# Performance work log

Hardware: AMD Instinct MI355X
Metric: run time of the kernel (lower is better)

Reference implementation:

```python
import jax, jax.numpy as jnp
import numpy as np

B, D = 16384, 512          # batch, outer_dim
S = R = O = X = Y = Z = 64  # inner tensor-network ranks


def _xavier(key, shape):
    fan_in, fan_out = shape[-2], shape[-1]
    if len(shape) == 3:
        fan_in = shape[0] * shape[1]
        fan_out = shape[2]
    limit = float(np.sqrt(6.0 / (fan_in + fan_out)))
    return jax.random.uniform(key, shape, jnp.float32, -limit, limit)


def setup_inputs() -> dict:
    key = jax.random.key(0)
    ks = jax.random.split(key, 12)
    return {
        "input1": jax.random.normal(ks[0], (B, D), jnp.float32),
        "input2": jax.random.normal(ks[1], (B, D), jnp.float32),
        "input3": jax.random.normal(ks[2], (B, D), jnp.float32),
        "proj_s": _xavier(ks[3], (D, S)),
        "proj_r": _xavier(ks[4], (R, R)),   # first_param = inn_r since with_nn
        "proj_o": _xavier(ks[5], (D, O)),
        "cube_s": _xavier(ks[6], (S, Y, Z)),
        "cube_r": _xavier(ks[7], (X, R, Z)),
        "cube_o": _xavier(ks[8], (X, Y, O)),
        "W21": _xavier(ks[9], (R, D)),
        "b21": jnp.zeros((R,), jnp.float32),
        "W22": _xavier(ks[10], (R, R)),
        "b22": jnp.zeros((R,), jnp.float32),
        "W23": _xavier(ks[11], (R, R)),
        "b23": jnp.zeros((R,), jnp.float32),
    }


def reference(input1, input2, input3, proj_s, proj_r, proj_o,
              cube_s, cube_r, cube_o, W21, b21, W22, b22, W23, b23):
    # relation MLP (with_nn=True branch)
    h = jax.nn.relu(input2 @ W21.T + b21)
    h = jax.nn.relu(h @ W22.T + b22)
    h = h @ W23.T + b23
    # projections: einsum('Ss,bS->bs', proj, x) == x @ proj
    p1 = input1 @ proj_s   # [B, S]
    p2 = h @ proj_r        # [B, R]
    p3 = input3 @ proj_o   # [B, O]
    # triangle contraction 'bs,br,bo,syz,xrz,xyo->b', contracted efficiently
    a = jnp.einsum('bs,syz->byz', p1, cube_s)
    b = jnp.einsum('br,xrz->bxz', p2, cube_r)
    c = jnp.einsum('bo,xyo->bxy', p3, cube_o)
    return jnp.einsum('byz,bxz,bxy->b', a, b, c)
```

## Files before the change

kernel.cpp:

```cpp
#include <hip/hip_runtime.h>
#include <hip/hip_bf16.h>
#include <cstdint>
#include <cstddef>


typedef __attribute__((ext_vector_type(8))) short short8;
typedef __attribute__((ext_vector_type(4))) float f32x4;

#define DEV static __device__ __forceinline__

constexpr int NB = 16384;
constexpr int ND = 512;

DEV unsigned short f2bf(float f) {
    union { float f; unsigned u; } v; v.f = f;
    unsigned r = v.u + 0x7FFFu + ((v.u >> 16) & 1u);
    return (unsigned short)(r >> 16);
}
DEV float bf2f(unsigned short h) {
    union { unsigned u; float f; } v; v.u = ((unsigned)h) << 16;
    return v.f;
}
DEV unsigned swz(unsigned byte_addr, int row) {
    return byte_addr ^ ((unsigned)(row & 7) << 4);
}

__global__ void k_prep(const float* __restrict__ proj_s, const float* __restrict__ proj_r,
                       const float* __restrict__ proj_o, const float* __restrict__ cube_s,
                       const float* __restrict__ cube_r, const float* __restrict__ cube_o,
                       const float* __restrict__ W21, const float* __restrict__ W22,
                       const float* __restrict__ W23,
                       unsigned short* __restrict__ Wp1t, unsigned short* __restrict__ Wh1,
                       unsigned short* __restrict__ Wp3t, unsigned short* __restrict__ W22b,
                       unsigned short* __restrict__ W23b, unsigned short* __restrict__ Prt,
                       unsigned short* __restrict__ csb, unsigned short* __restrict__ crb,
                       unsigned short* __restrict__ cot)
{
    int i = blockIdx.x * 256 + threadIdx.x;
    if (i < 32768) { int d = i >> 6, s = i & 63; Wp1t[s * 512 + d] = f2bf(proj_s[i]); return; }
    i -= 32768;
    if (i < 32768) { Wh1[i] = f2bf(W21[i]); return; }
    i -= 32768;
    if (i < 32768) { int d = i >> 6, o = i & 63; Wp3t[o * 512 + d] = f2bf(proj_o[i]); return; }
    i -= 32768;
    if (i < 4096) { W22b[i] = f2bf(W22[i]); return; }
    i -= 4096;
    if (i < 4096) { W23b[i] = f2bf(W23[i]); return; }
    i -= 4096;
    if (i < 4096) { int k = i >> 6, n = i & 63; Prt[n * 64 + k] = f2bf(proj_r[i]); return; }
    i -= 4096;
    if (i < 262144) { csb[i] = f2bf(cube_s[i]); return; }
    i -= 262144;
    if (i < 262144) { crb[i] = f2bf(cube_r[i]); return; }
    i -= 262144;
    if (i < 262144) { int x = i >> 12, y = (i >> 6) & 63, o = i & 63;
                      cot[o * 4096 + x * 64 + y] = f2bf(cube_o[i]); return; }
}

__global__ __launch_bounds__(256, 2) void k_proj(
    const float* __restrict__ in1, const float* __restrict__ in2, const float* __restrict__ in3,
    const unsigned short* __restrict__ Wp1t, const unsigned short* __restrict__ Wh1,
    const unsigned short* __restrict__ Wp3t, const float* __restrict__ b21,
    unsigned short* __restrict__ p1bf, unsigned short* __restrict__ hbf,
    unsigned short* __restrict__ p3bf)
{
    __shared__ __align__(16) unsigned short lds_w[64 * 512];
    __shared__ __align__(16) unsigned short lds_a[128 * 64];
    const int z = blockIdx.y;
    const float* in = (z == 0) ? in1 : (z == 1) ? in2 : in3;
    const unsigned short* Wt = (z == 0) ? Wp1t : (z == 1) ? Wh1 : Wp3t;
    unsigned short* outp = (z == 0) ? p1bf : (z == 1) ? hbf : p3bf;

    const int t = threadIdx.x;
    const int b0 = blockIdx.x * 128;

#pragma unroll
    for (int i = 0; i < 16; ++i) {
        int c = t + i * 256;
        int n = c >> 6, c16 = c & 63;
        uint4 v = *(const uint4*)(Wt + n * 512 + c16 * 8);
        *(uint4*)((char*)lds_w + swz(n * 1024 + c16 * 16, n)) = v;
    }
    const int wid = t >> 6, l = t & 63, lr = l & 15, lk = l >> 4;
    f32x4 acc[2][4] = {};
    for (int kc = 0; kc < 8; ++kc) {
#pragma unroll
        for (int i = 0; i < 4; ++i) {
            int u = t + i * 256;
            int row = u >> 3, e8 = u & 7;
            const float* src = in + (size_t)(b0 + row) * ND + kc * 64 + e8 * 8;
            float4 fa = *(const float4*)src;
            float4 fb = *(const float4*)(src + 4);
            uint4 pk;
            pk.x = (unsigned)f2bf(fa.x) | ((unsigned)f2bf(fa.y) << 16);
            pk.y = (unsigned)f2bf(fa.z) | ((unsigned)f2bf(fa.w) << 16);
            pk.z = (unsigned)f2bf(fb.x) | ((unsigned)f2bf(fb.y) << 16);
            pk.w = (unsigned)f2bf(fb.z) | ((unsigned)f2bf(fb.w) << 16);
            *(uint4*)((char*)lds_a + swz(row * 128 + e8 * 16, row)) = pk;
        }
        __syncthreads();
#pragma unroll
        for (int ks = 0; ks < 2; ++ks) {
            short8 av[2], bv[4];
#pragma unroll
            for (int f = 0; f < 2; ++f) {
                int row = wid * 32 + f * 16 + lr;
                av[f] = *(const short8*)((const char*)lds_a + swz(row * 128 + (ks * 32 + lk * 8) * 2, row));
            }
#pragma unroll
            for (int g = 0; g < 4; ++g) {
                int n = g * 16 + lr;
                bv[g] = *(const short8*)((const char*)lds_w + swz(n * 1024 + (kc * 64 + ks * 32 + lk * 8) * 2, n));
            }
#pragma unroll
            for (int f = 0; f < 2; ++f)
#pragma unroll
                for (int g = 0; g < 4; ++g)
                    acc[f][g] = __builtin_amdgcn_mfma_f32_16x16x32_bf16(av[f], bv[g], acc[f][g], 0, 0, 0);
        }
        __syncthreads();
    }
#pragma unroll
    for (int f = 0; f < 2; ++f)
#pragma unroll
        for (int g = 0; g < 4; ++g)
#pragma unroll
            for (int q = 0; q < 4; ++q) {
                int row = wid * 32 + f * 16 + lk * 4 + q;
                int col = g * 16 + lr;
                float v = acc[f][g][q];
                if (z == 1) v = fmaxf(v + b21[col], 0.0f);
                outp[(size_t)(b0 + row) * 64 + col] = f2bf(v);
            }
}

DEV void mlp_stage(const unsigned short* src_lds, const unsigned short* w_lds,
                   const float* __restrict__ bias, bool do_relu,
                   unsigned short* dst_lds, unsigned short* __restrict__ dst_g,
                   int b0, int wid, int lr, int lk)
{
    f32x4 acc[2][4] = {};
#pragma unroll
    for (int ks = 0; ks < 2; ++ks) {
        short8 av[2], bv[4];
#pragma unroll
        for (int f = 0; f < 2; ++f) {
            int row = wid * 32 + f * 16 + lr;
            av[f] = *(const short8*)((const char*)src_lds + swz(row * 128 + (ks * 32 + lk * 8) * 2, row));
        }
#pragma unroll
        for (int g = 0; g < 4; ++g) {
            int n = g * 16 + lr;
            bv[g] = *(const short8*)((const char*)w_lds + swz(n * 128 + (ks * 32 + lk * 8) * 2, n));
        }
#pragma unroll
        for (int f = 0; f < 2; ++f)
#pragma unroll
            for (int g = 0; g < 4; ++g)
                acc[f][g] = __builtin_amdgcn_mfma_f32_16x16x32_bf16(av[f], bv[g], acc[f][g], 0, 0, 0);
    }
#pragma unroll
    for (int f = 0; f < 2; ++f)
#pragma unroll
        for (int g = 0; g < 4; ++g)
#pragma unroll
            for (int q = 0; q < 4; ++q) {
                int row = wid * 32 + f * 16 + lk * 4 + q;
                int col = g * 16 + lr;
                float v = acc[f][g][q];
                if (bias) v += bias[col];
                if (do_relu) v = fmaxf(v, 0.0f);
                unsigned short hv = f2bf(v);
                if (dst_lds) *(unsigned short*)((char*)dst_lds + swz(row * 128 + col * 2, row)) = hv;
                else dst_g[(size_t)(b0 + row) * 64 + col] = hv;
            }
}

__global__ __launch_bounds__(256, 2) void k_mlp(
    const unsigned short* __restrict__ hbf,
    const unsigned short* __restrict__ W22b, const unsigned short* __restrict__ W23b,
    const unsigned short* __restrict__ Prt,
    const float* __restrict__ b22, const float* __restrict__ b23,
    unsigned short* __restrict__ p2bf)
{
    __shared__ __align__(16) unsigned short lds_w[3][64 * 64];
    __shared__ __align__(16) unsigned short lds_x[128 * 64];
    __shared__ __align__(16) unsigned short lds_y[128 * 64];
    const int t = threadIdx.x;
    const int b0 = blockIdx.x * 128;
#pragma unroll
    for (int i = 0; i < 6; ++i) {
        int c = t + i * 256;
        int w = c >> 9, cc = c & 511;
        int n = cc >> 3, c16 = cc & 7;
        const unsigned short* W = (w == 0) ? W22b : (w == 1) ? W23b : Prt;
        uint4 v = *(const uint4*)(W + n * 64 + c16 * 8);
        *(uint4*)((char*)lds_w[w] + swz(n * 128 + c16 * 16, n)) = v;
    }
#pragma unroll
    for (int i = 0; i < 4; ++i) {
        int u = t + i * 256;
        int row = u >> 3, c16 = u & 7;
        uint4 v = *(const uint4*)(hbf + (size_t)(b0 + row) * 64 + c16 * 8);
        *(uint4*)((char*)lds_x + swz(row * 128 + c16 * 16, row)) = v;
    }
    __syncthreads();
    const int wid = t >> 6, l = t & 63, lr = l & 15, lk = l >> 4;
    mlp_stage(lds_x, lds_w[0], b22, true,  lds_y, nullptr, b0, wid, lr, lk);
    __syncthreads();
    mlp_stage(lds_y, lds_w[1], b23, false, lds_x, nullptr, b0, wid, lr, lk);
    __syncthreads();
    mlp_stage(lds_x, lds_w[2], nullptr, false, nullptr, p2bf, b0, wid, lr, lk);
}

__global__ __launch_bounds__(256, 2) void k_F(
    const unsigned short* __restrict__ crb, const unsigned short* __restrict__ csb,
    unsigned short* __restrict__ F2)
{
    __shared__ __align__(16) unsigned short lds_a[128 * 64];
    __shared__ __align__(16) unsigned short lds_b[128 * 64];
    const int t = threadIdx.x;
    const int m0 = blockIdx.x * 128, n0 = blockIdx.y * 128;
#pragma unroll
    for (int i = 0; i < 4; ++i) {
        int u = t + i * 256;
        int row = u >> 3, c16 = u & 7;
        uint4 va = *(const uint4*)(crb + (size_t)(m0 + row) * 64 + c16 * 8);
        *(uint4*)((char*)lds_a + swz(row * 128 + c16 * 16, row)) = va;
        uint4 vb = *(const uint4*)(csb + (size_t)(n0 + row) * 64 + c16 * 8);
        *(uint4*)((char*)lds_b + swz(row * 128 + c16 * 16, row)) = vb;
    }
    __syncthreads();
    const int wid = t >> 6, l = t & 63, lr = l & 15, lk = l >> 4;
    const int wm = wid & 1, wn = wid >> 1;
    f32x4 acc[4][4] = {};
#pragma unroll
    for (int ks = 0; ks < 2; ++ks) {
        short8 av[4], bv[4];
#pragma unroll
        for (int f = 0; f < 4; ++f) {
            int row = wm * 64 + f * 16 + lr;
            av[f] = *(const short8*)((const char*)lds_a + swz(row * 128 + (ks * 32 + lk * 8) * 2, row));
            int col = wn * 64 + f * 16 + lr;
            bv[f] = *(const short8*)((const char*)lds_b + swz(col * 128 + (ks * 32 + lk * 8) * 2, col));
        }
#pragma unroll
        for (int f = 0; f < 4; ++f)
#pragma unroll
            for (int g = 0; g < 4; ++g)
                acc[f][g] = __builtin_amdgcn_mfma_f32_16x16x32_bf16(av[f], bv[g], acc[f][g], 0, 0, 0);
    }
#pragma unroll
    for (int f = 0; f < 4; ++f)
#pragma unroll
        for (int g = 0; g < 4; ++g)
#pragma unroll
            for (int q = 0; q < 4; ++q) {
                int row = m0 + wm * 64 + f * 16 + lk * 4 + q;
                int col = n0 + wn * 64 + g * 16 + lr;
                F2[(size_t)row * 4096 + col] = f2bf(acc[f][g][q]);
            }
}

__global__ __launch_bounds__(256, 1) void k_T(
    const unsigned short* __restrict__ F2, const unsigned short* __restrict__ cot,
    unsigned short* __restrict__ Tts)
{
    __shared__ __align__(16) unsigned short lds[4][2][64 * 64];
    const int s = blockIdx.x;
    const int t = threadIdx.x;
    const int wid = t >> 6, l = t & 63, lr = l & 15, lk = l >> 4;
    f32x4 acc[4][4] = {};
    for (int xi = 0; xi < 16; ++xi) {
        int x = wid * 16 + xi;
#pragma unroll
        for (int i = 0; i < 8; ++i) {
            int u = l + i * 64;
            int rr = u >> 3, c16 = u & 7;
            uint4 va = *(const uint4*)(F2 + (size_t)(x * 64 + rr) * 4096 + s * 64 + c16 * 8);
            *(uint4*)((char*)lds[wid][0] + swz(rr * 128 + c16 * 16, rr)) = va;
            uint4 vb = *(const uint4*)(cot + (size_t)rr * 4096 + x * 64 + c16 * 8);
            *(uint4*)((char*)lds[wid][1] + swz(rr * 128 + c16 * 16, rr)) = vb;
        }
        asm volatile("s_waitcnt lgkmcnt(0)" ::: "memory");
        __builtin_amdgcn_sched_barrier(0);
#pragma unroll
        for (int ks = 0; ks < 2; ++ks) {
            short8 av[4], bv[4];
#pragma unroll
            for (int f = 0; f < 4; ++f) {
                int rr = f * 16 + lr;
                av[f] = *(const short8*)((const char*)lds[wid][0] + swz(rr * 128 + (ks * 32 + lk * 8) * 2, rr));
                bv[f] = *(const short8*)((const char*)lds[wid][1] + swz(rr * 128 + (ks * 32 + lk * 8) * 2, rr));
            }
#pragma unroll
            for (int f = 0; f < 4; ++f)
#pragma unroll
                for (int g = 0; g < 4; ++g)
                    acc[f][g] = __builtin_amdgcn_mfma_f32_16x16x32_bf16(av[f], bv[g], acc[f][g], 0, 0, 0);
        }
    }
    __syncthreads();
    float* red = (float*)&lds[0][0][0];
#pragma unroll
    for (int f = 0; f < 4; ++f)
#pragma unroll
        for (int g = 0; g < 4; ++g)
#pragma unroll
            for (int q = 0; q < 4; ++q) {
                int r = f * 16 + lk * 4 + q;
                int o = g * 16 + lr;
                red[wid * 4096 + r * 64 + o] = acc[f][g][q];
            }
    __syncthreads();
#pragma unroll
    for (int i = 0; i < 16; ++i) {
        int idx = t + i * 256;
        float v = red[idx] + red[4096 + idx] + red[8192 + idx] + red[12288 + idx];
        Tts[(size_t)s * 4096 + idx] = f2bf(v);
    }
}

__global__ __launch_bounds__(256, 2) void k_main(
    const unsigned short* __restrict__ p1bf, const unsigned short* __restrict__ p2bf,
    const unsigned short* __restrict__ p3bf, const unsigned short* __restrict__ Tts,
    float* __restrict__ out)
{
    __shared__ __align__(16) unsigned short lds_t[64 * 64];
    __shared__ __align__(16) unsigned short lds_p2[128 * 64];
    __shared__ __align__(16) unsigned short lds_p3[128 * 64];
    const int t = threadIdx.x;
    const int b0 = blockIdx.x * 128;
    const int kh = blockIdx.y;
#pragma unroll
    for (int i = 0; i < 4; ++i) {
        int u = t + i * 256;
        int row = u >> 3, c16 = u & 7;
        uint4 v2 = *(const uint4*)(p2bf + (size_t)(b0 + row) * 64 + c16 * 8);
        *(uint4*)((char*)lds_p2 + swz(row * 128 + c16 * 16, row)) = v2;
        uint4 v3 = *(const uint4*)(p3bf + (size_t)(b0 + row) * 64 + c16 * 8);
        *(uint4*)((char*)lds_p3 + swz(row * 128 + c16 * 16, row)) = v3;
    }
    __syncthreads();
    const int wid = t >> 6, l = t & 63, lr = l & 15, lk = l >> 4;
    float p3v[2][2][8];
#pragma unroll
    for (int f = 0; f < 2; ++f)
#pragma unroll
        for (int ks = 0; ks < 2; ++ks) {
            int row = wid * 32 + f * 16 + lr;
            short8 v = *(const short8*)((const char*)lds_p3 + swz(row * 128 + (ks * 32 + lk * 8) * 2, row));
#pragma unroll
            for (int j = 0; j < 8; ++j) p3v[f][ks][j] = bf2f((unsigned short)v[j]);
        }
    f32x4 acc[2][4] = {};
    for (int kc = kh * 32; kc < kh * 32 + 32; ++kc) {
#pragma unroll
        for (int i = 0; i < 2; ++i) {
            int u = t + i * 256;
            int srow = u >> 3, c16 = u & 7;
            uint4 v = *(const uint4*)(Tts + (size_t)srow * 4096 + kc * 64 + c16 * 8);
            *(uint4*)((char*)lds_t + swz(srow * 128 + c16 * 16, srow)) = v;
        }
        __syncthreads();
        float p2v[2];
#pragma unroll
        for (int f = 0; f < 2; ++f) {
            int row = wid * 32 + f * 16 + lr;
            p2v[f] = bf2f(*(const unsigned short*)((const char*)lds_p2 + swz(row * 128 + kc * 2, row)));
        }
#pragma unroll
        for (int ks = 0; ks < 2; ++ks) {
            short8 av[2], bv[4];
#pragma unroll
            for (int f = 0; f < 2; ++f) {
                short8 a;
#pragma unroll
                for (int j = 0; j < 8; ++j) a[j] = (short)f2bf(p2v[f] * p3v[f][ks][j]);
                av[f] = a;
            }
#pragma unroll
            for (int g = 0; g < 4; ++g) {
                int n = g * 16 + lr;
                bv[g] = *(const short8*)((const char*)lds_t + swz(n * 128 + (ks * 32 + lk * 8) * 2, n));
            }
#pragma unroll
            for (int f = 0; f < 2; ++f)
#pragma unroll
                for (int g = 0; g < 4; ++g)
                    acc[f][g] = __builtin_amdgcn_mfma_f32_16x16x32_bf16(av[f], bv[g], acc[f][g], 0, 0, 0);
        }
        __syncthreads();
    }
    float rsum[2][4] = {};
#pragma unroll
    for (int f = 0; f < 2; ++f)
#pragma unroll
        for (int g = 0; g < 4; ++g)
#pragma unroll
            for (int q = 0; q < 4; ++q) {
                int row = wid * 32 + f * 16 + lk * 4 + q;
                int col = g * 16 + lr;
                float p1v = bf2f(p1bf[(size_t)(b0 + row) * 64 + col]);
                rsum[f][q] += acc[f][g][q] * p1v;
            }
#pragma unroll
    for (int f = 0; f < 2; ++f)
#pragma unroll
        for (int q = 0; q < 4; ++q) {
            float v = rsum[f][q];
            v += __shfl_xor(v, 1);
            v += __shfl_xor(v, 2);
            v += __shfl_xor(v, 4);
            v += __shfl_xor(v, 8);
            if (lr == 0) {
                int row = wid * 32 + f * 16 + lk * 4 + q;
                atomicAdd(&out[b0 + row], v);
            }
        }
}

extern "C" void kernel_launch(void* const* d_in, const int* in_sizes, int n_in,
                              void* d_out, int out_size, void* d_ws, size_t ws_size,
                              hipStream_t stream)
{
    const float* in1    = (const float*)d_in[0];
    const float* in2    = (const float*)d_in[1];
    const float* in3    = (const float*)d_in[2];
    const float* proj_s = (const float*)d_in[3];
    const float* proj_r = (const float*)d_in[4];
    const float* proj_o = (const float*)d_in[5];
    const float* cube_s = (const float*)d_in[6];
    const float* cube_r = (const float*)d_in[7];
    const float* cube_o = (const float*)d_in[8];
    const float* W21    = (const float*)d_in[9];
    const float* b21    = (const float*)d_in[10];
    const float* W22    = (const float*)d_in[11];
    const float* b22    = (const float*)d_in[12];
    const float* W23    = (const float*)d_in[13];
    const float* b23    = (const float*)d_in[14];
    float* out = (float*)d_out;

    char* ws = (char*)d_ws;
    size_t off = 0;
    auto alloc = [&](size_t bytes) -> char* {
        char* p = ws + off;
        off += (bytes + 255) & ~(size_t)255;
        return p;
    };
    unsigned short* p1bf = (unsigned short*)alloc((size_t)NB * 64 * 2);
    unsigned short* hbf  = (unsigned short*)alloc((size_t)NB * 64 * 2);
    unsigned short* p2bf = (unsigned short*)alloc((size_t)NB * 64 * 2);
    unsigned short* p3bf = (unsigned short*)alloc((size_t)NB * 64 * 2);
    unsigned short* Wp1t = (unsigned short*)alloc(64 * 512 * 2);
    unsigned short* Wh1  = (unsigned short*)alloc(64 * 512 * 2);
    unsigned short* Wp3t = (unsigned short*)alloc(64 * 512 * 2);
    unsigned short* W22b = (unsigned short*)alloc(64 * 64 * 2);
    unsigned short* W23b = (unsigned short*)alloc(64 * 64 * 2);
    unsigned short* Prt  = (unsigned short*)alloc(64 * 64 * 2);
    unsigned short* csb  = (unsigned short*)alloc(262144 * 2);
    unsigned short* crb  = (unsigned short*)alloc(262144 * 2);
    unsigned short* cot  = (unsigned short*)alloc(262144 * 2);
    unsigned short* Tts  = (unsigned short*)alloc(64 * 4096 * 2);
    unsigned short* F2   = (unsigned short*)alloc((size_t)4096 * 4096 * 2);

    hipMemsetAsync(d_out, 0, (size_t)out_size * sizeof(float), stream);

    k_prep<<<3504, 256, 0, stream>>>(proj_s, proj_r, proj_o, cube_s, cube_r, cube_o,
                                     W21, W22, W23,
                                     Wp1t, Wh1, Wp3t, W22b, W23b, Prt, csb, crb, cot);
    k_proj<<<dim3(NB / 128, 3), 256, 0, stream>>>(in1, in2, in3, Wp1t, Wh1, Wp3t, b21,
                                                  p1bf, hbf, p3bf);
    k_mlp<<<NB / 128, 256, 0, stream>>>(hbf, W22b, W23b, Prt, b22, b23, p2bf);
    k_F<<<dim3(32, 32), 256, 0, stream>>>(crb, csb, F2);
    k_T<<<64, 256, 0, stream>>>(F2, cot, Tts);
    k_main<<<dim3(NB / 128, 2), 256, 0, stream>>>(p1bf, p2bf, p3bf, Tts, out);
}
```

Measured before the change: 236.0 us.

## Fuse MLP into projection kernel, split T across x-chunks, double-buffer main kernel

```diff
diff --git a/kernel.cpp b/kernel.cpp
--- a/kernel.cpp
+++ b/kernel.cpp
@@ -21,19 +21,24 @@
     union { unsigned u; float f; } v; v.u = ((unsigned)h) << 16;
     return v.f;
 }
-DEV unsigned swz(unsigned byte_addr, int row) {
-    return byte_addr ^ ((unsigned)(row & 7) << 4);
+DEV unsigned pack2(float lo, float hi) {
+    return (unsigned)f2bf(lo) | ((unsigned)f2bf(hi) << 16);
+}
+DEV short8 ldA_f32(const float* p) {
+    float4 a = *(const float4*)p, b = *(const float4*)(p + 4);
+    union { unsigned u[4]; short8 s; } v;
+    v.u[0] = pack2(a.x, a.y); v.u[1] = pack2(a.z, a.w);
+    v.u[2] = pack2(b.x, b.y); v.u[3] = pack2(b.z, b.w);
+    return v.s;
 }
 
 __global__ void k_prep(const float* __restrict__ proj_s, const float* __restrict__ proj_r,
-                       const float* __restrict__ proj_o, const float* __restrict__ cube_s,
-                       const float* __restrict__ cube_r, const float* __restrict__ cube_o,
+                       const float* __restrict__ proj_o, const float* __restrict__ cube_o,
                        const float* __restrict__ W21, const float* __restrict__ W22,
                        const float* __restrict__ W23,
                        unsigned short* __restrict__ Wp1t, unsigned short* __restrict__ Wh1,
                        unsigned short* __restrict__ Wp3t, unsigned short* __restrict__ W22b,
                        unsigned short* __restrict__ W23b, unsigned short* __restrict__ Prt,
-                       unsigned short* __restrict__ csb, unsigned short* __restrict__ crb,
                        unsigned short* __restrict__ cot)
 {
     int i = blockIdx.x * 256 + threadIdx.x;
@@ -49,375 +54,267 @@
     i -= 4096;
     if (i < 4096) { int k = i >> 6, n = i & 63; Prt[n * 64 + k] = f2bf(proj_r[i]); return; }
     i -= 4096;
-    if (i < 262144) { csb[i] = f2bf(cube_s[i]); return; }
-    i -= 262144;
-    if (i < 262144) { crb[i] = f2bf(cube_r[i]); return; }
-    i -= 262144;
     if (i < 262144) { int x = i >> 12, y = (i >> 6) & 63, o = i & 63;
                       cot[o * 4096 + x * 64 + y] = f2bf(cube_o[i]); return; }
+}
+
+__global__ __launch_bounds__(256, 2) void k_F(
+    const float* __restrict__ cr, const float* __restrict__ cs,
+    unsigned short* __restrict__ F2)
+{
+    const int t = threadIdx.x, wid = t >> 6, l = t & 63, lr = l & 15, lk = l >> 4;
+    const int wm = wid & 1, wn = wid >> 1;
+    const int m0 = blockIdx.x * 128 + wm * 64, n0 = blockIdx.y * 128 + wn * 64;
+    f32x4 acc[4][4] = {};
+#pragma unroll
+    for (int ks = 0; ks < 2; ++ks) {
+        short8 av[4], bv[4];
+#pragma unroll
+        for (int f = 0; f < 4; ++f) {
+            av[f] = ldA_f32(cr + (size_t)(m0 + f * 16 + lr) * 64 + ks * 32 + lk * 8);
+            bv[f] = ldA_f32(cs + (size_t)(n0 + f * 16 + lr) * 64 + ks * 32 + lk * 8);
+        }
+#pragma unroll
+        for (int f = 0; f < 4; ++f)
+#pragma unroll
+            for (int g = 0; g < 4; ++g)
+                acc[f][g] = __builtin_amdgcn_mfma_f32_16x16x32_bf16(av[f], bv[g], acc[f][g], 0, 0, 0);
+    }
+#pragma unroll
+    for (int f = 0; f < 4; ++f)
+#pragma unroll
+        for (int g = 0; g < 4; ++g)
+#pragma unroll
+            for (int q = 0; q < 4; ++q)
+                F2[(size_t)(m0 + f * 16 + lk * 4 + q) * 4096 + n0 + g * 16 + lr] = f2bf(acc[f][g][q]);
+}
+
+DEV void mlp_mm(const unsigned short* slab_w, const unsigned short* __restrict__ W,
+                int lr, int lk, f32x4 acc[4])
+{
+#pragma unroll
+    for (int ks = 0; ks < 2; ++ks) {
+        short8 av = *(const short8*)((const char*)slab_w +
+                      (lr * 128 + ((ks * 64 + lk * 16) ^ ((lr & 7) << 4))));
+#pragma unroll
+        for (int g = 0; g < 4; ++g) {
+            short8 bv = *(const short8*)(W + (g * 16 + lr) * 64 + ks * 32 + lk * 8);
+            acc[g] = __builtin_amdgcn_mfma_f32_16x16x32_bf16(av, bv, acc[g], 0, 0, 0);
+        }
+    }
+}
+DEV void store_slab(unsigned short* slab_w, int lr, int lk, const f32x4 acc[4],
+                    const float* __restrict__ bias, bool relu_)
+{
+#pragma unroll
+    for (int g = 0; g < 4; ++g) {
+        float bcol = bias ? bias[g * 16 + lr] : 0.0f;
+#pragma unroll
+        for (int q = 0; q < 4; ++q) {
+            int r = lk * 4 + q, c = g * 16 + lr;
+            float v = acc[g][q] + bcol;
+            if (relu_) v = fmaxf(v, 0.0f);
+            *(unsigned short*)((char*)slab_w + (r * 128 + ((c * 2) ^ ((r & 7) << 4)))) = f2bf(v);
+        }
+    }
 }
 
 __global__ __launch_bounds__(256, 2) void k_proj(
     const float* __restrict__ in1, const float* __restrict__ in2, const float* __restrict__ in3,
     const unsigned short* __restrict__ Wp1t, const unsigned short* __restrict__ Wh1,
-    const unsigned short* __restrict__ Wp3t, const float* __restrict__ b21,
-    unsigned short* __restrict__ p1bf, unsigned short* __restrict__ hbf,
+    const unsigned short* __restrict__ Wp3t,
+    const unsigned short* __restrict__ W22b, const unsigned short* __restrict__ W23b,
+    const unsigned short* __restrict__ Prt,
+    const float* __restrict__ b21, const float* __restrict__ b22, const float* __restrict__ b23,
+    unsigned short* __restrict__ p1bf, unsigned short* __restrict__ p2bf,
     unsigned short* __restrict__ p3bf)
 {
-    __shared__ __align__(16) unsigned short lds_w[64 * 512];
-    __shared__ __align__(16) unsigned short lds_a[128 * 64];
+    __shared__ __align__(16) unsigned short slab[4][1024];
     const int z = blockIdx.y;
     const float* in = (z == 0) ? in1 : (z == 1) ? in2 : in3;
     const unsigned short* Wt = (z == 0) ? Wp1t : (z == 1) ? Wh1 : Wp3t;
-    unsigned short* outp = (z == 0) ? p1bf : (z == 1) ? hbf : p3bf;
-
-    const int t = threadIdx.x;
-    const int b0 = blockIdx.x * 128;
-
-#pragma unroll
-    for (int i = 0; i < 16; ++i) {
-        int c = t + i * 256;
-        int n = c >> 6, c16 = c & 63;
-        uint4 v = *(const uint4*)(Wt + n * 512 + c16 * 8);
-        *(uint4*)((char*)lds_w + swz(n * 1024 + c16 * 16, n)) = v;
-    }
-    const int wid = t >> 6, l = t & 63, lr = l & 15, lk = l >> 4;
-    f32x4 acc[2][4] = {};
+    const int t = threadIdx.x, wid = t >> 6, l = t & 63, lr = l & 15, lk = l >> 4;
+    const int rbase = blockIdx.x * 64 + wid * 16;
+    const float* arow = in + (size_t)(rbase + lr) * ND;
+
+    f32x4 acc[4] = {};
+#pragma unroll
     for (int kc = 0; kc < 8; ++kc) {
 #pragma unroll
-        for (int i = 0; i < 4; ++i) {
-            int u = t + i * 256;
-            int row = u >> 3, e8 = u & 7;
-            const float* src = in + (size_t)(b0 + row) * ND + kc * 64 + e8 * 8;
-            float4 fa = *(const float4*)src;
-            float4 fb = *(const float4*)(src + 4);
-            uint4 pk;
-            pk.x = (unsigned)f2bf(fa.x) | ((unsigned)f2bf(fa.y) << 16);
-            pk.y = (unsigned)f2bf(fa.z) | ((unsigned)f2bf(fa.w) << 16);
-            pk.z = (unsigned)f2bf(fb.x) | ((unsigned)f2bf(fb.y) << 16);
-            pk.w = (unsigned)f2bf(fb.z) | ((unsigned)f2bf(fb.w) << 16);
-            *(uint4*)((char*)lds_a + swz(row * 128 + e8 * 16, row)) = pk;
-        }
+        for (int ks = 0; ks < 2; ++ks) {
+            short8 av = ldA_f32(arow + kc * 64 + ks * 32 + lk * 8);
+#pragma unroll
+            for (int g = 0; g < 4; ++g) {
+                short8 bv = *(const short8*)(Wt + (size_t)(g * 16 + lr) * 512 + kc * 64 + ks * 32 + lk * 8);
+                acc[g] = __builtin_amdgcn_mfma_f32_16x16x32_bf16(av, bv, acc[g], 0, 0, 0);
+            }
+        }
+    }
+    if (z != 1) {
+        unsigned short* outp = (z == 0) ? p1bf : p3bf;
+#pragma unroll
+        for (int g = 0; g < 4; ++g)
+#pragma unroll
+            for (int q = 0; q < 4; ++q)
+                outp[(size_t)(rbase + lk * 4 + q) * 64 + g * 16 + lr] = f2bf(acc[g][q]);
+    } else {
+        unsigned short* slw = slab[wid];
+        store_slab(slw, lr, lk, acc, b21, true);
         __syncthreads();
+        f32x4 a2[4] = {}; mlp_mm(slw, W22b, lr, lk, a2);
+        store_slab(slw, lr, lk, a2, b22, true);
+        __syncthreads();
+        f32x4 a3[4] = {}; mlp_mm(slw, W23b, lr, lk, a3);
+        store_slab(slw, lr, lk, a3, b23, false);
+        __syncthreads();
+        f32x4 a4[4] = {}; mlp_mm(slw, Prt, lr, lk, a4);
+#pragma unroll
+        for (int g = 0; g < 4; ++g)
+#pragma unroll
+            for (int q = 0; q < 4; ++q)
+                p2bf[(size_t)(rbase + lk * 4 + q) * 64 + g * 16 + lr] = f2bf(a4[g][q]);
+    }
+}
+
+__global__ __launch_bounds__(256, 2) void k_T(
+    const unsigned short* __restrict__ F2, const unsigned short* __restrict__ cot,
+    float* __restrict__ Tf)
+{
+    __shared__ float red[4][4096];
+    const int s = blockIdx.x, xh = blockIdx.y;
+    const int t = threadIdx.x, wid = t >> 6, l = t & 63, lr = l & 15, lk = l >> 4;
+    f32x4 acc[4][4] = {};
+#pragma unroll
+    for (int xi = 0; xi < 4; ++xi) {
+        int x = xh * 16 + wid * 4 + xi;
 #pragma unroll
         for (int ks = 0; ks < 2; ++ks) {
-            short8 av[2], bv[4];
-#pragma unroll
-            for (int f = 0; f < 2; ++f) {
-                int row = wid * 32 + f * 16 + lr;
-                av[f] = *(const short8*)((const char*)lds_a + swz(row * 128 + (ks * 32 + lk * 8) * 2, row));
+            short8 av[4], bv[4];
+#pragma unroll
+            for (int f = 0; f < 4; ++f) {
+                av[f] = *(const short8*)(F2 + (size_t)(x * 64 + f * 16 + lr) * 4096 + s * 64 + ks * 32 + lk * 8);
+                bv[f] = *(const short8*)(cot + (size_t)(f * 16 + lr) * 4096 + x * 64 + ks * 32 + lk * 8);
             }
 #pragma unroll
-            for (int g = 0; g < 4; ++g) {
-                int n = g * 16 + lr;
-                bv[g] = *(const short8*)((const char*)lds_w + swz(n * 1024 + (kc * 64 + ks * 32 + lk * 8) * 2, n));
-            }
-#pragma unroll
-            for (int f = 0; f < 2; ++f)
+            for (int f = 0; f < 4; ++f)
 #pragma unroll
                 for (int g = 0; g < 4; ++g)
                     acc[f][g] = __builtin_amdgcn_mfma_f32_16x16x32_bf16(av[f], bv[g], acc[f][g], 0, 0, 0);
         }
-        __syncthreads();
-    }
-#pragma unroll
-    for (int f = 0; f < 2; ++f)
+    }
+#pragma unroll
+    for (int f = 0; f < 4; ++f)
 #pragma unroll
         for (int g = 0; g < 4; ++g)
 #pragma unroll
-            for (int q = 0; q < 4; ++q) {
-                int row = wid * 32 + f * 16 + lk * 4 + q;
-                int col = g * 16 + lr;
-                float v = acc[f][g][q];
-                if (z == 1) v = fmaxf(v + b21[col], 0.0f);
-                outp[(size_t)(b0 + row) * 64 + col] = f2bf(v);
-            }
-}
-
-DEV void mlp_stage(const unsigned short* src_lds, const unsigned short* w_lds,
-                   const float* __restrict__ bias, bool do_relu,
-                   unsigned short* dst_lds, unsigned short* __restrict__ dst_g,
-                   int b0, int wid, int lr, int lk)
-{
-    f32x4 acc[2][4] = {};
-#pragma unroll
-    for (int ks = 0; ks < 2; ++ks) {
-        short8 av[2], bv[4];
-#pragma unroll
-        for (int f = 0; f < 2; ++f) {
-            int row = wid * 32 + f * 16 + lr;
-            av[f] = *(const short8*)((const char*)src_lds + swz(row * 128 + (ks * 32 + lk * 8) * 2, row));
-        }
-#pragma unroll
-        for (int g = 0; g < 4; ++g) {
-            int n = g * 16 + lr;
-            bv[g] = *(const short8*)((const char*)w_lds + swz(n * 128 + (ks * 32 + lk * 8) * 2, n));
-        }
-#pragma unroll
-        for (int f = 0; f < 2; ++f)
-#pragma unroll
-            for (int g = 0; g < 4; ++g)
-                acc[f][g] = __builtin_amdgcn_mfma_f32_16x16x32_bf16(av[f], bv[g], acc[f][g], 0, 0, 0);
-    }
-#pragma unroll
-    for (int f = 0; f < 2; ++f)
-#pragma unroll
-        for (int g = 0; g < 4; ++g)
-#pragma unroll
-            for (int q = 0; q < 4; ++q) {
-                int row = wid * 32 + f * 16 + lk * 4 + q;
-                int col = g * 16 + lr;
-                float v = acc[f][g][q];
-                if (bias) v += bias[col];
-                if (do_relu) v = fmaxf(v, 0.0f);
-                unsigned short hv = f2bf(v);
-                if (dst_lds) *(unsigned short*)((char*)dst_lds + swz(row * 128 + col * 2, row)) = hv;
-                else dst_g[(size_t)(b0 + row) * 64 + col] = hv;
-            }
-}
-
-__global__ __launch_bounds__(256, 2) void k_mlp(
-    const unsigned short* __restrict__ hbf,
-    const unsigned short* __restrict__ W22b, const unsigned short* __restrict__ W23b,
-    const unsigned short* __restrict__ Prt,
-    const float* __restrict__ b22, const float* __restrict__ b23,
-    unsigned short* __restrict__ p2bf)
-{
-    __shared__ __align__(16) unsigned short lds_w[3][64 * 64];
-    __shared__ __align__(16) unsigned short lds_x[128 * 64];
-    __shared__ __align__(16) unsigned short lds_y[128 * 64];
-    const int t = threadIdx.x;
-    const int b0 = blockIdx.x * 128;
-#pragma unroll
-    for (int i = 0; i < 6; ++i) {
-        int c = t + i * 256;
-        int w = c >> 9, cc = c & 511;
-        int n = cc >> 3, c16 = cc & 7;
-        const unsigned short* W = (w == 0) ? W22b : (w == 1) ? W23b : Prt;
-        uint4 v = *(const uint4*)(W + n * 64 + c16 * 8);
-        *(uint4*)((char*)lds_w[w] + swz(n * 128 + c16 * 16, n)) = v;
-    }
-#pragma unroll
-    for (int i = 0; i < 4; ++i) {
-        int u = t + i * 256;
-        int row = u >> 3, c16 = u & 7;
-        uint4 v = *(const uint4*)(hbf + (size_t)(b0 + row) * 64 + c16 * 8);
-        *(uint4*)((char*)lds_x + swz(row * 128 + c16 * 16, row)) = v;
-    }
-    __syncthreads();
-    const int wid = t >> 6, l = t & 63, lr = l & 15, lk = l >> 4;
-    mlp_stage(lds_x, lds_w[0], b22, true,  lds_y, nullptr, b0, wid, lr, lk);
-    __syncthreads();
-    mlp_stage(lds_y, lds_w[1], b23, false, lds_x, nullptr, b0, wid, lr, lk);
-    __syncthreads();
-    mlp_stage(lds_x, lds_w[2], nullptr, false, nullptr, p2bf, b0, wid, lr, lk);
-}
-
-__global__ __launch_bounds__(256, 2) void k_F(
-    const unsigned short* __restrict__ crb, const unsigned short* __restrict__ csb,
-    unsigned short* __restrict__ F2)
-{
-    __shared__ __align__(16) unsigned short lds_a[128 * 64];
-    __shared__ __align__(16) unsigned short lds_b[128 * 64];
-    const int t = threadIdx.x;
-    const int m0 = blockIdx.x * 128, n0 = blockIdx.y * 128;
-#pragma unroll
-    for (int i = 0; i < 4; ++i) {
-        int u = t + i * 256;
-        int row = u >> 3, c16 = u & 7;
-        uint4 va = *(const uint4*)(crb + (size_t)(m0 + row) * 64 + c16 * 8);
-        *(uint4*)((char*)lds_a + swz(row * 128 + c16 * 16, row)) = va;
-        uint4 vb = *(const uint4*)(csb + (size_t)(n0 + row) * 64 + c16 * 8);
-        *(uint4*)((char*)lds_b + swz(row * 128 + c16 * 16, row)) = vb;
-    }
-    __syncthreads();
-    const int wid = t >> 6, l = t & 63, lr = l & 15, lk = l >> 4;
-    const int wm = wid & 1, wn = wid >> 1;
-    f32x4 acc[4][4] = {};
-#pragma unroll
-    for (int ks = 0; ks < 2; ++ks) {
-        short8 av[4], bv[4];
-#pragma unroll
-        for (int f = 0; f < 4; ++f) {
-            int row = wm * 64 + f * 16 + lr;
-            av[f] = *(const short8*)((const char*)lds_a + swz(row * 128 + (ks * 32 + lk * 8) * 2, row));
-            int col = wn * 64 + f * 16 + lr;
-            bv[f] = *(const short8*)((const char*)lds_b + swz(col * 128 + (ks * 32 + lk * 8) * 2, col));
-        }
-#pragma unroll
-        for (int f = 0; f < 4; ++f)
-#pragma unroll
-            for (int g = 0; g < 4; ++g)
-                acc[f][g] = __builtin_amdgcn_mfma_f32_16x16x32_bf16(av[f], bv[g], acc[f][g], 0, 0, 0);
-    }
-#pragma unroll
-    for (int f = 0; f < 4; ++f)
-#pragma unroll
-        for (int g = 0; g < 4; ++g)
-#pragma unroll
-            for (int q = 0; q < 4; ++q) {
-                int row = m0 + wm * 64 + f * 16 + lk * 4 + q;
-                int col = n0 + wn * 64 + g * 16 + lr;
-                F2[(size_t)row * 4096 + col] = f2bf(acc[f][g][q]);
-            }
-}
-
-__global__ __launch_bounds__(256, 1) void k_T(
-    const unsigned short* __restrict__ F2, const unsigned short* __restrict__ cot,
-    unsigned short* __restrict__ Tts)
-{
-    __shared__ __align__(16) unsigned short lds[4][2][64 * 64];
-    const int s = blockIdx.x;
-    const int t = threadIdx.x;
-    const int wid = t >> 6, l = t & 63, lr = l & 15, lk = l >> 4;
-    f32x4 acc[4][4] = {};
-    for (int xi = 0; xi < 16; ++xi) {
-        int x = wid * 16 + xi;
-#pragma unroll
-        for (int i = 0; i < 8; ++i) {
-            int u = l + i * 64;
-            int rr = u >> 3, c16 = u & 7;
-            uint4 va = *(const uint4*)(F2 + (size_t)(x * 64 + rr) * 4096 + s * 64 + c16 * 8);
-            *(uint4*)((char*)lds[wid][0] + swz(rr * 128 + c16 * 16, rr)) = va;
-            uint4 vb = *(const uint4*)(cot + (size_t)rr * 4096 + x * 64 + c16 * 8);
-            *(uint4*)((char*)lds[wid][1] + swz(rr * 128 + c16 * 16, rr)) = vb;
-        }
-        asm volatile("s_waitcnt lgkmcnt(0)" ::: "memory");
-        __builtin_amdgcn_sched_barrier(0);
-#pragma unroll
-        for (int ks = 0; ks < 2; ++ks) {
-            short8 av[4], bv[4];
-#pragma unroll
-            for (int f = 0; f < 4; ++f) {
-                int rr = f * 16 + lr;
-                av[f] = *(const short8*)((const char*)lds[wid][0] + swz(rr * 128 + (ks * 32 + lk * 8) * 2, rr));
-                bv[f] = *(const short8*)((const char*)lds[wid][1] + swz(rr * 128 + (ks * 32 + lk * 8) * 2, rr));
-            }
-#pragma unroll
-            for (int f = 0; f < 4; ++f)
-#pragma unroll
-                for (int g = 0; g < 4; ++g)
-                    acc[f][g] = __builtin_amdgcn_mfma_f32_16x16x32_bf16(av[f], bv[g], acc[f][g], 0, 0, 0);
-        }
-    }
-    __syncthreads();
-    float* red = (float*)&lds[0][0][0];
-#pragma unroll
-    for (int f = 0; f < 4; ++f)
-#pragma unroll
-        for (int g = 0; g < 4; ++g)
-#pragma unroll
-            for (int q = 0; q < 4; ++q) {
-                int r = f * 16 + lk * 4 + q;
-                int o = g * 16 + lr;
-                red[wid * 4096 + r * 64 + o] = acc[f][g][q];
-            }
+            for (int q = 0; q < 4; ++q)
+                red[wid][(f * 16 + lk * 4 + q) * 64 + g * 16 + lr] = acc[f][g][q];
     __syncthreads();
 #pragma unroll
     for (int i = 0; i < 16; ++i) {
         int idx = t + i * 256;
-        float v = red[idx] + red[4096 + idx] + red[8192 + idx] + red[12288 + idx];
-        Tts[(size_t)s * 4096 + idx] = f2bf(v);
-    }
-}
-
-__global__ __launch_bounds__(256, 2) void k_main(
+        atomicAdd(&Tf[(size_t)s * 4096 + idx],
+                  red[0][idx] + red[1][idx] + red[2][idx] + red[3][idx]);
+    }
+}
+
+__global__ void k_cast(const float* __restrict__ Tf, unsigned short* __restrict__ Tts)
+{
+    int i = blockIdx.x * 256 + threadIdx.x;
+#pragma unroll
+    for (int j = 0; j < 4; ++j) {
+        int e = i * 4 + j;
+        int s = e >> 12, k = e & 4095;
+        int kc = k >> 6, kloc = k & 63;
+        Tts[kc * 4096 + s * 64 + kloc] = f2bf(Tf[e]);
+    }
+}
+
+__global__ __launch_bounds__(256, 4) void k_main(
     const unsigned short* __restrict__ p1bf, const unsigned short* __restrict__ p2bf,
     const unsigned short* __restrict__ p3bf, const unsigned short* __restrict__ Tts,
     float* __restrict__ out)
 {
-    __shared__ __align__(16) unsigned short lds_t[64 * 64];
-    __shared__ __align__(16) unsigned short lds_p2[128 * 64];
-    __shared__ __align__(16) unsigned short lds_p3[128 * 64];
-    const int t = threadIdx.x;
-    const int b0 = blockIdx.x * 128;
-    const int kh = blockIdx.y;
-#pragma unroll
-    for (int i = 0; i < 4; ++i) {
-        int u = t + i * 256;
-        int row = u >> 3, c16 = u & 7;
-        uint4 v2 = *(const uint4*)(p2bf + (size_t)(b0 + row) * 64 + c16 * 8);
-        *(uint4*)((char*)lds_p2 + swz(row * 128 + c16 * 16, row)) = v2;
-        uint4 v3 = *(const uint4*)(p3bf + (size_t)(b0 + row) * 64 + c16 * 8);
-        *(uint4*)((char*)lds_p3 + swz(row * 128 + c16 * 16, row)) = v3;
-    }
-    __syncthreads();
-    const int wid = t >> 6, l = t & 63, lr = l & 15, lk = l >> 4;
-    float p3v[2][2][8];
-#pragma unroll
-    for (int f = 0; f < 2; ++f)
+    __shared__ __align__(16) unsigned short tb[2][4096];
+    const int t = threadIdx.x, wid = t >> 6, l = t & 63, lr = l & 15, lk = l >> 4;
+    const int b0 = blockIdx.x * 64, kh = blockIdx.y;
+    const int row = b0 + wid * 16 + lr;
+
+    float p3v[2][8];
+#pragma unroll
+    for (int ks = 0; ks < 2; ++ks) {
+        short8 v = *(const short8*)(p3bf + (size_t)row * 64 + ks * 32 + lk * 8);
+#pragma unroll
+        for (int j = 0; j < 8; ++j) p3v[ks][j] = bf2f((unsigned short)v[j]);
+    }
+    short8 p2r[2];
+#pragma unroll
+    for (int i = 0; i < 2; ++i)
+        p2r[i] = *(const short8*)(p2bf + (size_t)row * 64 + kh * 16 + i * 8);
+
+    const int srow_st = t >> 2, kb_st = (t & 3) * 32;
+    const unsigned swz0 = (unsigned)(kb_st ^ ((srow_st & 7) << 4));
+    const unsigned swz1 = (unsigned)((kb_st + 16) ^ ((srow_st & 7) << 4));
+
+    {
+        const uint4* src = (const uint4*)((const char*)(Tts + (size_t)(kh * 16) * 4096) + t * 32);
+        uint4 v0 = src[0], v1 = src[1];
+        char* dst = (char*)tb[0] + srow_st * 128;
+        *(uint4*)(dst + swz0) = v0;
+        *(uint4*)(dst + swz1) = v1;
+        __syncthreads();
+    }
+
+    f32x4 acc[4] = {};
+#pragma unroll
+    for (int i = 0; i < 16; ++i) {
+        const int buf = i & 1;
+        uint4 n0 = {}, n1 = {};
+        if (i < 15) {
+            const uint4* src = (const uint4*)((const char*)(Tts + (size_t)(kh * 16 + i + 1) * 4096) + t * 32);
+            n0 = src[0]; n1 = src[1];
+        }
+        float p2s = bf2f((unsigned short)p2r[i >> 3][i & 7]);
 #pragma unroll
         for (int ks = 0; ks < 2; ++ks) {
-            int row = wid * 32 + f * 16 + lr;
-            short8 v = *(const short8*)((const char*)lds_p3 + swz(row * 128 + (ks * 32 + lk * 8) * 2, row));
-#pragma unroll
-            for (int j = 0; j < 8; ++j) p3v[f][ks][j] = bf2f((unsigned short)v[j]);
-        }
-    f32x4 acc[2][4] = {};
-    for (int kc = kh * 32; kc < kh * 32 + 32; ++kc) {
-#pragma unroll
-        for (int i = 0; i < 2; ++i) {
-            int u = t + i * 256;
-            int srow = u >> 3, c16 = u & 7;
-            uint4 v = *(const uint4*)(Tts + (size_t)srow * 4096 + kc * 64 + c16 * 8);
-            *(uint4*)((char*)lds_t + swz(srow * 128 + c16 * 16, srow)) = v;
-        }
-        __syncthreads();
-        float p2v[2];
-#pragma unroll
-        for (int f = 0; f < 2; ++f) {
-            int row = wid * 32 + f * 16 + lr;
-            p2v[f] = bf2f(*(const unsigned short*)((const char*)lds_p2 + swz(row * 128 + kc * 2, row)));
-        }
-#pragma unroll
-        for (int ks = 0; ks < 2; ++ks) {
-            short8 av[2], bv[4];
-#pragma unroll
-            for (int f = 0; f < 2; ++f) {
-                short8 a;
-#pragma unroll
-                for (int j = 0; j < 8; ++j) a[j] = (short)f2bf(p2v[f] * p3v[f][ks][j]);
-                av[f] = a;
-            }
+            union { unsigned u[4]; short8 s; } a;
+#pragma unroll
+            for (int jj = 0; jj < 4; ++jj)
+                a.u[jj] = pack2(p2s * p3v[ks][jj * 2], p2s * p3v[ks][jj * 2 + 1]);
 #pragma unroll
             for (int g = 0; g < 4; ++g) {
                 int n = g * 16 + lr;
-                bv[g] = *(const short8*)((const char*)lds_t + swz(n * 128 + (ks * 32 + lk * 8) * 2, n));
+                short8 bv = *(const short8*)((const char*)tb[buf] +
+                              (n * 128 + ((ks * 64 + lk * 16) ^ ((n & 7) << 4))));
+                acc[g] = __builtin_amdgcn_mfma_f32_16x16x32_bf16(a.s, bv, acc[g], 0, 0, 0);
             }
-#pragma unroll
-            for (int f = 0; f < 2; ++f)
-#pragma unroll
-                for (int g = 0; g < 4; ++g)
-                    acc[f][g] = __builtin_amdgcn_mfma_f32_16x16x32_bf16(av[f], bv[g], acc[f][g], 0, 0, 0);
-        }
-        __syncthreads();
-    }
-    float rsum[2][4] = {};
-#pragma unroll
-    for (int f = 0; f < 2; ++f)
-#pragma unroll
-        for (int g = 0; g < 4; ++g)
-#pragma unroll
-            for (int q = 0; q < 4; ++q) {
-                int row = wid * 32 + f * 16 + lk * 4 + q;
-                int col = g * 16 + lr;
-                float p1v = bf2f(p1bf[(size_t)(b0 + row) * 64 + col]);
-                rsum[f][q] += acc[f][g][q] * p1v;
-            }
-#pragma unroll
-    for (int f = 0; f < 2; ++f)
+        }
+        if (i < 15) {
+            char* dst = (char*)tb[buf ^ 1] + srow_st * 128;
+            *(uint4*)(dst + swz0) = n0;
+            *(uint4*)(dst + swz1) = n1;
+            __syncthreads();
+        }
+    }
+
+    float rsum[4] = {};
+#pragma unroll
+    for (int g = 0; g < 4; ++g)
 #pragma unroll
         for (int q = 0; q < 4; ++q) {
-            float v = rsum[f][q];
-            v += __shfl_xor(v, 1);
-            v += __shfl_xor(v, 2);
-            v += __shfl_xor(v, 4);
-            v += __shfl_xor(v, 8);
-            if (lr == 0) {
-                int row = wid * 32 + f * 16 + lk * 4 + q;
-                atomicAdd(&out[b0 + row], v);
-            }
-        }
+            int r = b0 + wid * 16 + lk * 4 + q, c = g * 16 + lr;
+            rsum[q] += acc[g][q] * bf2f(p1bf[(size_t)r * 64 + c]);
+        }
+#pragma unroll
+    for (int q = 0; q < 4; ++q) {
+        float v = rsum[q];
+        v += __shfl_xor(v, 1);
+        v += __shfl_xor(v, 2);
+        v += __shfl_xor(v, 4);
+        v += __shfl_xor(v, 8);
+        if (lr == 0)
+            atomicAdd(&out[b0 + wid * 16 + lk * 4 + q], v);
+    }
 }
 
 extern "C" void kernel_launch(void* const* d_in, const int* in_sizes, int n_in,
@@ -449,7 +346,6 @@
         return p;
     };
     unsigned short* p1bf = (unsigned short*)alloc((size_t)NB * 64 * 2);
-    unsigned short* hbf  = (unsigned short*)alloc((size_t)NB * 64 * 2);
     unsigned short* p2bf = (unsigned short*)alloc((size_t)NB * 64 * 2);
     unsigned short* p3bf = (unsigned short*)alloc((size_t)NB * 64 * 2);
     unsigned short* Wp1t = (unsigned short*)alloc(64 * 512 * 2);
@@ -458,21 +354,21 @@
     unsigned short* W22b = (unsigned short*)alloc(64 * 64 * 2);
     unsigned short* W23b = (unsigned short*)alloc(64 * 64 * 2);
     unsigned short* Prt  = (unsigned short*)alloc(64 * 64 * 2);
-    unsigned short* csb  = (unsigned short*)alloc(262144 * 2);
-    unsigned short* crb  = (unsigned short*)alloc(262144 * 2);
     unsigned short* cot  = (unsigned short*)alloc(262144 * 2);
-    unsigned short* Tts  = (unsigned short*)alloc(64 * 4096 * 2);
+    float*          Tf   = (float*)alloc(262144 * 4);
+    unsigned short* Tts  = (unsigned short*)alloc(262144 * 2);
     unsigned short* F2   = (unsigned short*)alloc((size_t)4096 * 4096 * 2);
 
     hipMemsetAsync(d_out, 0, (size_t)out_size * sizeof(float), stream);
-
-    k_prep<<<3504, 256, 0, stream>>>(proj_s, proj_r, proj_o, cube_s, cube_r, cube_o,
-                                     W21, W22, W23,
-                                     Wp1t, Wh1, Wp3t, W22b, W23b, Prt, csb, crb, cot);
-    k_proj<<<dim3(NB / 128, 3), 256, 0, stream>>>(in1, in2, in3, Wp1t, Wh1, Wp3t, b21,
-                                                  p1bf, hbf, p3bf);
-    k_mlp<<<NB / 128, 256, 0, stream>>>(hbf, W22b, W23b, Prt, b22, b23, p2bf);
-    k_F<<<dim3(32, 32), 256, 0, stream>>>(crb, csb, F2);
-    k_T<<<64, 256, 0, stream>>>(F2, cot, Tts);
-    k_main<<<dim3(NB / 128, 2), 256, 0, stream>>>(p1bf, p2bf, p3bf, Tts, out);
-}
+    hipMemsetAsync(Tf, 0, 262144 * sizeof(float), stream);
+
+    k_prep<<<1456, 256, 0, stream>>>(proj_s, proj_r, proj_o, cube_o, W21, W22, W23,
+                                     Wp1t, Wh1, Wp3t, W22b, W23b, Prt, cot);
+    k_F<<<dim3(32, 32), 256, 0, stream>>>(cube_r, cube_s, F2);
+    k_proj<<<dim3(NB / 64, 3), 256, 0, stream>>>(in1, in2, in3, Wp1t, Wh1, Wp3t,
+                                                 W22b, W23b, Prt, b21, b22, b23,
+                                                 p1bf, p2bf, p3bf);
+    k_T<<<dim3(64, 4), 256, 0, stream>>>(F2, cot, Tf);
+    k_cast<<<256, 256, 0, stream>>>(Tf, Tts);
+    k_main<<<dim3(NB / 64, 4), 256, 0, stream>>>(p1bf, p2bf, p3bf, Tts, out);
+}
```

After: 228.9 us. 3.0% less time.
